# Kernel optimization log

Hardware: AMD Instinct MI355X
Metric: run time of the kernel (lower is better)

Reference implementation:

```python
import jax, jax.numpy as jnp
import numpy as np

EPS = 1e-6
TOP_K = 2


def setup_inputs() -> dict:
    key = jax.random.key(0)
    k0, k1, k2, k3, k4 = jax.random.split(key, 5)
    B, S, H, I, E = 1, 2048, 1024, 3584, 8
    return {
        "hidden_states": jax.random.normal(k0, (B, S, H), jnp.float32),
        "rms_weight": jnp.ones((H,), jnp.float32),
        "gate_w": jax.random.normal(k1, (E, H), jnp.float32) * (H ** -0.5),
        "w1": jax.random.normal(k2, (E, I, H), jnp.float32) * (H ** -0.5),
        "w2": jax.random.normal(k3, (E, H, I), jnp.float32) * (I ** -0.5),
        "w3": jax.random.normal(k4, (E, I, H), jnp.float32) * (H ** -0.5),
    }


def reference(hidden_states, rms_weight, gate_w, w1, w2, w3):
    B, S, H = hidden_states.shape
    E = gate_w.shape[0]
    # RMSNorm (fp32 internally, matches _RMSNorm)
    x = hidden_states.astype(jnp.float32)
    var = jnp.mean(x * x, axis=-1, keepdims=True)
    h = rms_weight * (x * jax.lax.rsqrt(var + EPS))  # [B,S,H]
    # Router: softmax over experts, top-k, renormalize
    logits = jnp.einsum('bsh,eh->bse', h, gate_w)
    scores = jax.nn.softmax(logits.astype(jnp.float32), axis=-1)
    top_w, top_i = jax.lax.top_k(scores, TOP_K)        # [B,S,K]
    top_w = top_w / jnp.sum(top_w, axis=-1, keepdims=True)
    top_w = top_w.astype(h.dtype)
    # Per-token combine weight for every expert: cw[t,e]
    hf = h.reshape(-1, H)                               # [T,H]
    oh = jax.nn.one_hot(top_i.reshape(-1, TOP_K), E, dtype=h.dtype)  # [T,K,E]
    cw = jnp.einsum('tke,tk->te', oh, top_w.reshape(-1, TOP_K))       # [T,E]
    # SwiGLU expert MLPs, batched over experts (dense dispatch; weights zero out unrouted tokens)
    a = jnp.einsum('th,eih->eti', hf, w1)               # [E,T,I]
    g = jnp.einsum('th,eih->eti', hf, w3)               # [E,T,I]
    eo = jnp.einsum('eti,ehi->eth', jax.nn.silu(a) * g, w2)  # [E,T,H]
    out = jnp.einsum('eth,te->th', eo, cw)              # [T,H]
    return hidden_states + out.reshape(B, S, H)
```

## Files before the change

### kernel.cpp

```cpp
#include <hip/hip_runtime.h>
#include <hip/hip_bf16.h>
#include <stdint.h>

#define T_TOK 2048
#define HDIM  1024
#define IDIM  3584
#define NEXP  8
#define NROWS 4096
#define WELEM 29360128

typedef __attribute__((ext_vector_type(8))) short bf16x8;
typedef __attribute__((ext_vector_type(4))) float f32x4;
typedef __attribute__((ext_vector_type(4))) unsigned int u32x4;

typedef __attribute__((address_space(3))) unsigned lds_u32;
typedef const __attribute__((address_space(1))) unsigned glb_u32;

#define MFMA16 __builtin_amdgcn_mfma_f32_16x16x32_bf16

__device__ __forceinline__ unsigned short f2bf(float f){
  union { float f; unsigned u; } v; v.f = f;
  unsigned r = v.u + 0x7FFFu + ((v.u >> 16) & 1u);
  return (unsigned short)(r >> 16);
}
__device__ __forceinline__ unsigned cvt2(float a, float b){
  __hip_bfloat162 h = __float22bfloat162_rn(float2{a, b});
  return *reinterpret_cast<unsigned*>(&h);
}
__device__ __forceinline__ bf16x8 pack8(float4 lo, float4 hi){
  union { __hip_bfloat162 b2[4]; bf16x8 v; } u;
  u.b2[0] = __float22bfloat162_rn(float2{lo.x, lo.y});
  u.b2[1] = __float22bfloat162_rn(float2{lo.z, lo.w});
  u.b2[2] = __float22bfloat162_rn(float2{hi.x, hi.y});
  u.b2[3] = __float22bfloat162_rn(float2{hi.z, hi.w});
  return u.v;
}

__global__ __launch_bounds__(256) void k_rms_router(
    const float* __restrict__ x, const float* __restrict__ rmsw,
    const float* __restrict__ gw, unsigned short* __restrict__ h_bf,
    int* __restrict__ topk_i, float* __restrict__ topk_w, int* __restrict__ count)
{
  const int t = blockIdx.x, tid = threadIdx.x;
  const int lane = tid & 63, wid = tid >> 6;
  float4 x4 = reinterpret_cast<const float4*>(x)[t*256 + tid];
  float ss = x4.x*x4.x + x4.y*x4.y + x4.z*x4.z + x4.w*x4.w;
  #pragma unroll
  for (int o = 32; o >= 1; o >>= 1) ss += __shfl_xor(ss, o);
  __shared__ float sred[4];
  __shared__ float slog[32];
  if (lane == 0) sred[wid] = ss;
  __syncthreads();
  float inv = rsqrtf((sred[0]+sred[1]+sred[2]+sred[3]) * (1.0f/HDIM) + 1e-6f);
  float4 w4 = reinterpret_cast<const float4*>(rmsw)[tid];
  float h0 = x4.x*inv*w4.x, h1 = x4.y*inv*w4.y, h2 = x4.z*inv*w4.z, h3 = x4.w*inv*w4.w;
  ushort4 hb; hb.x = f2bf(h0); hb.y = f2bf(h1); hb.z = f2bf(h2); hb.w = f2bf(h3);
  reinterpret_cast<ushort4*>(h_bf)[t*256 + tid] = hb;
  #pragma unroll
  for (int e = 0; e < NEXP; e++){
    float4 g4 = reinterpret_cast<const float4*>(gw)[e*256 + tid];
    float v = h0*g4.x + h1*g4.y + h2*g4.z + h3*g4.w;
    #pragma unroll
    for (int o = 32; o >= 1; o >>= 1) v += __shfl_xor(v, o);
    if (lane == 0) slog[e*4 + wid] = v;
  }
  __syncthreads();
  if (tid == 0){
    float lg[NEXP];
    #pragma unroll
    for (int e = 0; e < NEXP; e++) lg[e] = slog[e*4]+slog[e*4+1]+slog[e*4+2]+slog[e*4+3];
    int i0 = 0;
    for (int e = 1; e < NEXP; e++) if (lg[e] > lg[i0]) i0 = e;
    int i1 = -1;
    for (int e = 0; e < NEXP; e++){ if (e == i0) continue; if (i1 < 0 || lg[e] > lg[i1]) i1 = e; }
    float m  = fmaxf(lg[i0], lg[i1]);
    float e0 = expf(lg[i0]-m), e1 = expf(lg[i1]-m);
    float s  = e0 + e1;
    topk_i[t*2] = i0; topk_i[t*2+1] = i1;
    topk_w[t*2] = e0/s; topk_w[t*2+1] = e1/s;
    atomicAdd(&count[i0], 1); atomicAdd(&count[i1], 1);
  }
}

__global__ void k_scan(const int* __restrict__ count, int* __restrict__ offset){
  if (threadIdx.x == 0){
    int o = 0;
    for (int e = 0; e < NEXP; e++){ offset[e] = o; o += count[e]; }
  }
}

__global__ __launch_bounds__(256) void k_scatter(
    const int* __restrict__ topk_i, const float* __restrict__ topk_w,
    const int* __restrict__ offset, int* __restrict__ cursor,
    int* __restrict__ token_of_row, float* __restrict__ wrow, int* __restrict__ slot_of)
{
  int t = blockIdx.x*256 + threadIdx.x;
  if (t >= T_TOK) return;
  #pragma unroll
  for (int k = 0; k < 2; k++){
    int e = topk_i[t*2+k];
    int pos = atomicAdd(&cursor[e], 1);
    int row = offset[e] + pos;
    token_of_row[row] = t;
    wrow[row] = topk_w[t*2+k];
    slot_of[t*2+k] = row;
  }
}

__global__ __launch_bounds__(256) void k_cvt(
    const float4* __restrict__ src, uint2* __restrict__ dst, int n4)
{
  int stride = gridDim.x * blockDim.x;
  for (int i = blockIdx.x*blockDim.x + threadIdx.x; i < n4; i += stride){
    float4 v = src[i];
    dst[i] = make_uint2(cvt2(v.x, v.y), cvt2(v.z, v.w));
  }
}

__global__ __launch_bounds__(256, 3) void k_mlp_in_bf(
    const unsigned short* __restrict__ h_bf, const unsigned short* __restrict__ w1bf,
    const unsigned short* __restrict__ w3bf, const int* __restrict__ token_of_row,
    const int* __restrict__ count, const int* __restrict__ offset,
    unsigned short* __restrict__ act)
{
  const int d = blockIdx.x;
  const int e = d & 7;
  const int q = d >> 3;
  const int panel = q >> 4;
  const int rt = q & 15;
  const int cnt = count[e];
  if (rt * 128 >= cnt) return;
  const int off = offset[e], row0 = off + rt*128, rend = off + cnt;
  const int col0 = panel * 64;
  const int tid = threadIdx.x, lane = tid & 63, wid = tid >> 6;
  const int wave_r = wid >> 1, wave_c = wid & 1;

  __shared__ __align__(16) char sA [128*128];
  __shared__ __align__(16) char sB1[64*128];
  __shared__ __align__(16) char sB2[64*128];

  const int srow = tid >> 3;
  const int sg   = (tid & 7) ^ (srow & 7);

  const unsigned short* aptr[4];
  #pragma unroll
  for (int j = 0; j < 4; j++){
    int tok = token_of_row[min(row0 + srow + 32*j, NROWS-1)];
    aptr[j] = h_bf + (size_t)tok*HDIM + sg*8;
  }
  const unsigned short* b1ptr[2];
  const unsigned short* b3ptr[2];
  #pragma unroll
  for (int j = 0; j < 2; j++){
    int col = col0 + srow + 32*j;
    b1ptr[j] = w1bf + (size_t)(e*IDIM + col)*HDIM + sg*8;
    b3ptr[j] = w3bf + (size_t)(e*IDIM + col)*HDIM + sg*8;
  }

  #define ISSUE(kk) {                                                                \
    _Pragma("unroll")                                                                \
    for (int j = 0; j < 4; j++)                                                      \
      __builtin_amdgcn_global_load_lds((glb_u32*)(const void*)(aptr[j] + (kk)*64),   \
          (lds_u32*)(void*)(sA + j*4096 + tid*16), 16, 0, 0);                        \
    _Pragma("unroll")                                                                \
    for (int j = 0; j < 2; j++){                                                     \
      __builtin_amdgcn_global_load_lds((glb_u32*)(const void*)(b1ptr[j] + (kk)*64),  \
          (lds_u32*)(void*)(sB1 + j*4096 + tid*16), 16, 0, 0);                       \
      __builtin_amdgcn_global_load_lds((glb_u32*)(const void*)(b3ptr[j] + (kk)*64),  \
          (lds_u32*)(void*)(sB2 + j*4096 + tid*16), 16, 0, 0);                       \
    } }

  f32x4 acc1[4][2], acc3[4][2];
  #pragma unroll
  for (int m = 0; m < 4; m++)
    #pragma unroll
    for (int n = 0; n < 2; n++){
      acc1[m][n] = (f32x4){0.f,0.f,0.f,0.f};
      acc3[m][n] = (f32x4){0.f,0.f,0.f,0.f};
    }

  for (int kk = 0; kk < HDIM/64; kk++){
    ISSUE(kk);
    __syncthreads();
    #pragma unroll
    for (int ki = 0; ki < 2; ki++){
      bf16x8 af[4];
      #pragma unroll
      for (int m = 0; m < 4; m++){
        int row = wave_r*64 + m*16 + (lane & 15);
        int slot = ki*4 + (lane >> 4);
        af[m] = *reinterpret_cast<const bf16x8*>(sA + row*128 + ((slot ^ (row&7))<<4));
      }
      #pragma unroll
      for (int n = 0; n < 2; n++){
        int col = wave_c*32 + n*16 + (lane & 15);
        int slot = ki*4 + (lane >> 4);
        bf16x8 b1 = *reinterpret_cast<const bf16x8*>(sB1 + col*128 + ((slot ^ (col&7))<<4));
        bf16x8 b2 = *reinterpret_cast<const bf16x8*>(sB2 + col*128 + ((slot ^ (col&7))<<4));
        #pragma unroll
        for (int m = 0; m < 4; m++){
          acc1[m][n] = MFMA16(af[m], b1, acc1[m][n], 0,0,0);
          acc3[m][n] = MFMA16(af[m], b2, acc3[m][n], 0,0,0);
        }
      }
    }
    __syncthreads();
  }

  const int lcol = lane & 15, lrow4 = (lane >> 4) * 4;
  #pragma unroll
  for (int m = 0; m < 4; m++){
    #pragma unroll
    for (int n = 0; n < 2; n++){
      int gcol = col0 + wave_c*32 + n*16 + lcol;
      #pragma unroll
      for (int r = 0; r < 4; r++){
        int grow = row0 + wave_r*64 + m*16 + lrow4 + r;
        if (grow < rend){
          float a = acc1[m][n][r], g = acc3[m][n][r];
          float sig = 1.0f / (1.0f + __expf(-a));
          act[(size_t)grow*IDIM + gcol] = f2bf(a * sig * g);
        }
      }
    }
  }
  #undef ISSUE
}

__global__ __launch_bounds__(256, 4) void k_mlp_out_bf(
    const unsigned short* __restrict__ act, const unsigned short* __restrict__ w2bf,
    const float* __restrict__ wrow, const int* __restrict__ count,
    const int* __restrict__ offset, float* __restrict__ eo)
{
  const int d = blockIdx.x;
  const int e = d & 7;
  const int q = d >> 3;
  const int panel = q >> 4;
  const int rt = q & 15;
  const int cnt = count[e];
  if (rt * 128 >= cnt) return;
  const int off = offset[e], row0 = off + rt*128, rend = off + cnt;
  const int col0 = panel * 64;
  const int tid = threadIdx.x, lane = tid & 63, wid = tid >> 6;
  const int wave_r = wid >> 1, wave_c = wid & 1;

  __shared__ __align__(16) char sA[128*128];
  __shared__ __align__(16) char sB[64*128];

  const int srow = tid >> 3;
  const int sg   = (tid & 7) ^ (srow & 7);

  const unsigned short* aptr[4];
  #pragma unroll
  for (int j = 0; j < 4; j++){
    int r = min(row0 + srow + 32*j, NROWS-1);
    aptr[j] = act + (size_t)r*IDIM + sg*8;
  }
  const unsigned short* bptr[2];
  #pragma unroll
  for (int j = 0; j < 2; j++){
    int col = col0 + srow + 32*j;
    bptr[j] = w2bf + (size_t)(e*HDIM + col)*IDIM + sg*8;
  }

  #define ISSUE(kk) {                                                                \
    _Pragma("unroll")                                                                \
    for (int j = 0; j < 4; j++)                                                      \
      __builtin_amdgcn_global_load_lds((glb_u32*)(const void*)(aptr[j] + (kk)*64),   \
          (lds_u32*)(void*)(sA + j*4096 + tid*16), 16, 0, 0);                        \
    _Pragma("unroll")                                                                \
    for (int j = 0; j < 2; j++)                                                      \
      __builtin_amdgcn_global_load_lds((glb_u32*)(const void*)(bptr[j] + (kk)*64),   \
          (lds_u32*)(void*)(sB + j*4096 + tid*16), 16, 0, 0); }

  f32x4 acc[4][2];
  #pragma unroll
  for (int m = 0; m < 4; m++)
    #pragma unroll
    for (int n = 0; n < 2; n++) acc[m][n] = (f32x4){0.f,0.f,0.f,0.f};

  for (int kk = 0; kk < IDIM/64; kk++){
    ISSUE(kk);
    __syncthreads();
    #pragma unroll
    for (int ki = 0; ki < 2; ki++){
      bf16x8 af[4];
      #pragma unroll
      for (int m = 0; m < 4; m++){
        int row = wave_r*64 + m*16 + (lane & 15);
        int slot = ki*4 + (lane >> 4);
        af[m] = *reinterpret_cast<const bf16x8*>(sA + row*128 + ((slot ^ (row&7))<<4));
      }
      #pragma unroll
      for (int n = 0; n < 2; n++){
        int col = wave_c*32 + n*16 + (lane & 15);
        int slot = ki*4 + (lane >> 4);
        bf16x8 fb = *reinterpret_cast<const bf16x8*>(sB + col*128 + ((slot ^ (col&7))<<4));
        #pragma unroll
        for (int m = 0; m < 4; m++)
          acc[m][n] = MFMA16(af[m], fb, acc[m][n], 0,0,0);
      }
    }
    __syncthreads();
  }

  const int lcol = lane & 15, lrow4 = (lane >> 4) * 4;
  #pragma unroll
  for (int m = 0; m < 4; m++){
    #pragma unroll
    for (int n = 0; n < 2; n++){
      int gcol = col0 + wave_c*32 + n*16 + lcol;
      #pragma unroll
      for (int r = 0; r < 4; r++){
        int grow = row0 + wave_r*64 + m*16 + lrow4 + r;
        if (grow < rend){
          eo[(size_t)grow*HDIM + gcol] = acc[m][n][r] * wrow[grow];
        }
      }
    }
  }
  #undef ISSUE
}

__global__ __launch_bounds__(256, 2) void k_mlp_in_fb(
    const unsigned short* __restrict__ h_bf, const float* __restrict__ w1,
    const float* __restrict__ w3, const int* __restrict__ token_of_row,
    const int* __restrict__ count, const int* __restrict__ offset,
    unsigned short* __restrict__ act)
{
  int bx, by, bz;
  {
    int d = blockIdx.x + 16*(blockIdx.y + 56*blockIdx.z);
    int w = (d & 7)*896 + (d >> 3);
    bx = w & 15; int r = w >> 4; by = r % 56; bz = r / 56;
  }
  const int e = bz, tile = bx;
  const int cnt = count[e];
  if (tile * 128 >= cnt) return;
  const int off  = offset[e];
  const int row0 = off + tile*128;
  const int rend = off + cnt;
  const int col0 = by * 64;
  const int tid = threadIdx.x, lane = tid & 63, wid = tid >> 6;
  const int wave_r = wid >> 1, wave_c = wid & 1;

  __shared__ __align__(16) char sA [128*128];
  __shared__ __align__(16) char sB1[64*128];
  __shared__ __align__(16) char sB2[64*128];

  const int arow_base = tid >> 3;
  const int kseg = tid & 7;
  const unsigned short* aptr[4];
  #pragma unroll
  for (int j = 0; j < 4; j++){
    int r = row0 + arow_base + 32*j;
    aptr[j] = h_bf + (size_t)token_of_row[min(r, NROWS-1)]*HDIM + kseg*8;
  }
  const float* w1base = w1 + (size_t)e*IDIM*HDIM + (size_t)col0*HDIM + (size_t)arow_base*HDIM + kseg*8;
  const float* w3base = w3 + (size_t)e*IDIM*HDIM + (size_t)col0*HDIM + (size_t)arow_base*HDIM + kseg*8;

  u32x4  pa[4];
  float4 pb1[2][2], pb3[2][2];

  auto LOAD = [&](int kk){
    #pragma unroll
    for (int j = 0; j < 4; j++)
      pa[j] = *reinterpret_cast<const u32x4*>(aptr[j] + kk*64);
    #pragma unroll
    for (int j = 0; j < 2; j++){
      const float4* p1 = reinterpret_cast<const float4*>(w1base + (size_t)(32*j)*HDIM + kk*64);
      const float4* p3 = reinterpret_cast<const float4*>(w3base + (size_t)(32*j)*HDIM + kk*64);
      pb1[j][0] = p1[0]; pb1[j][1] = p1[1];
      pb3[j][0] = p3[0]; pb3[j][1] = p3[1];
    }
  };
  const int aswz = (kseg ^ (arow_base & 7)) << 4;
  auto STORE = [&](){
    #pragma unroll
    for (int j = 0; j < 4; j++)
      *reinterpret_cast<u32x4*>(sA + (arow_base + 32*j)*128 + aswz) = pa[j];
    #pragma unroll
    for (int j = 0; j < 2; j++){
      *reinterpret_cast<bf16x8*>(sB1 + (arow_base + 32*j)*128 + aswz) = pack8(pb1[j][0], pb1[j][1]);
      *reinterpret_cast<bf16x8*>(sB2 + (arow_base + 32*j)*128 + aswz) = pack8(pb3[j][0], pb3[j][1]);
    }
  };

  f32x4 acc_a[4][2], acc_g[4][2];
  #pragma unroll
  for (int m = 0; m < 4; m++)
    #pragma unroll
    for (int n = 0; n < 2; n++){
      acc_a[m][n] = (f32x4){0.f,0.f,0.f,0.f};
      acc_g[m][n] = (f32x4){0.f,0.f,0.f,0.f};
    }

  LOAD(0);
  for (int kk = 0; kk < HDIM/64; kk++){
    STORE();
    if (kk + 1 < HDIM/64) LOAD(kk+1);
    __syncthreads();
    #pragma unroll
    for (int ki = 0; ki < 2; ki++){
      bf16x8 af[4];
      #pragma unroll
      for (int m = 0; m < 4; m++){
        int row = wave_r*64 + m*16 + (lane&15);
        int slot = ki*4 + (lane>>4);
        af[m] = *reinterpret_cast<const bf16x8*>(sA + row*128 + ((slot ^ (row&7))<<4));
      }
      #pragma unroll
      for (int n = 0; n < 2; n++){
        int col = wave_c*32 + n*16 + (lane&15);
        int slot = ki*4 + (lane>>4);
        bf16x8 b1 = *reinterpret_cast<const bf16x8*>(sB1 + col*128 + ((slot ^ (col&7))<<4));
        bf16x8 b2 = *reinterpret_cast<const bf16x8*>(sB2 + col*128 + ((slot ^ (col&7))<<4));
        #pragma unroll
        for (int m = 0; m < 4; m++){
          acc_a[m][n] = MFMA16(af[m], b1, acc_a[m][n], 0,0,0);
          acc_g[m][n] = MFMA16(af[m], b2, acc_g[m][n], 0,0,0);
        }
      }
    }
    __syncthreads();
  }
  const int lcol = lane & 15, lrow4 = (lane >> 4) * 4;
  #pragma unroll
  for (int m = 0; m < 4; m++){
    #pragma unroll
    for (int n = 0; n < 2; n++){
      int gcol = col0 + wave_c*32 + n*16 + lcol;
      #pragma unroll
      for (int r = 0; r < 4; r++){
        int grow = row0 + wave_r*64 + m*16 + lrow4 + r;
        if (grow < rend){
          float a = acc_a[m][n][r], g = acc_g[m][n][r];
          float sig = 1.0f / (1.0f + __expf(-a));
          act[(size_t)grow*IDIM + gcol] = f2bf(a * sig * g);
        }
      }
    }
  }
}

__global__ __launch_bounds__(256, 3) void k_mlp_out_fb(
    const unsigned short* __restrict__ act, const float* __restrict__ w2,
    const float* __restrict__ wrow, const int* __restrict__ count,
    const int* __restrict__ offset, float* __restrict__ eo)
{
  int bx, by, bz;
  {
    int d = blockIdx.x + 16*(blockIdx.y + 16*blockIdx.z);
    int w = (d & 7)*256 + (d >> 3);
    bx = w & 15; int r = w >> 4; by = r & 15; bz = r >> 4;
  }
  const int e = bz, tile = bx;
  const int cnt = count[e];
  if (tile*128 >= cnt) return;
  const int off = offset[e], row0 = off + tile*128, rend = off + cnt;
  const int col0 = by * 64;
  const int tid = threadIdx.x, lane = tid & 63, wid = tid >> 6;
  const int wave_r = wid >> 1, wave_c = wid & 1;

  __shared__ __align__(16) char sA[128*128];
  __shared__ __align__(16) char sB[64*128];

  const int arow_base = tid >> 3, kseg = tid & 7;
  const unsigned short* aptr[4];
  #pragma unroll
  for (int j = 0; j < 4; j++){
    int r = min(row0 + arow_base + 32*j, NROWS-1);
    aptr[j] = act + (size_t)r * IDIM + kseg*8;
  }
  const float* w2base = w2 + (size_t)e*HDIM*IDIM + (size_t)col0*IDIM + (size_t)arow_base*IDIM + kseg*8;

  u32x4  pa[4];
  float4 pb[2][2];

  auto LOAD = [&](int kk){
    #pragma unroll
    for (int j = 0; j < 4; j++)
      pa[j] = *reinterpret_cast<const u32x4*>(aptr[j] + kk*64);
    #pragma unroll
    for (int j = 0; j < 2; j++){
      const float4* p = reinterpret_cast<const float4*>(w2base + (size_t)(32*j)*IDIM + kk*64);
      pb[j][0] = p[0]; pb[j][1] = p[1];
    }
  };
  const int aswz = (kseg ^ (arow_base & 7)) << 4;
  auto STORE = [&](){
    #pragma unroll
    for (int j = 0; j < 4; j++)
      *reinterpret_cast<u32x4*>(sA + (arow_base + 32*j)*128 + aswz) = pa[j];
    #pragma unroll
    for (int j = 0; j < 2; j++)
      *reinterpret_cast<bf16x8*>(sB + (arow_base + 32*j)*128 + aswz) = pack8(pb[j][0], pb[j][1]);
  };

  f32x4 acc[4][2];
  #pragma unroll
  for (int m = 0; m < 4; m++)
    #pragma unroll
    for (int n = 0; n < 2; n++) acc[m][n] = (f32x4){0.f,0.f,0.f,0.f};

  LOAD(0);
  for (int kk = 0; kk < IDIM/64; kk++){
    STORE();
    if (kk + 1 < IDIM/64) LOAD(kk+1);
    __syncthreads();
    #pragma unroll
    for (int ki = 0; ki < 2; ki++){
      bf16x8 af[4];
      #pragma unroll
      for (int m = 0; m < 4; m++){
        int row = wave_r*64 + m*16 + (lane&15);
        int slot = ki*4 + (lane>>4);
        af[m] = *reinterpret_cast<const bf16x8*>(sA + row*128 + ((slot ^ (row&7))<<4));
      }
      #pragma unroll
      for (int n = 0; n < 2; n++){
        int col = wave_c*32 + n*16 + (lane&15);
        int slot = ki*4 + (lane>>4);
        bf16x8 fb = *reinterpret_cast<const bf16x8*>(sB + col*128 + ((slot ^ (col&7))<<4));
        #pragma unroll
        for (int m = 0; m < 4; m++)
          acc[m][n] = MFMA16(af[m], fb, acc[m][n], 0,0,0);
      }
    }
    __syncthreads();
  }
  const int lcol = lane & 15, lrow4 = (lane >> 4) * 4;
  #pragma unroll
  for (int m = 0; m < 4; m++){
    #pragma unroll
    for (int n = 0; n < 2; n++){
      int gcol = col0 + wave_c*32 + n*16 + lcol;
      #pragma unroll
      for (int r = 0; r < 4; r++){
        int grow = row0 + wave_r*64 + m*16 + lrow4 + r;
        if (grow < rend){
          eo[(size_t)grow*HDIM + gcol] = acc[m][n][r] * wrow[grow];
        }
      }
    }
  }
}

__global__ __launch_bounds__(256) void k_combine(
    const float* __restrict__ x, const float* __restrict__ eo,
    const int* __restrict__ slot_of, float* __restrict__ out)
{
  const int t = blockIdx.x, tid = threadIdx.x;
  const int s0 = slot_of[t*2], s1 = slot_of[t*2+1];
  float4 xv = reinterpret_cast<const float4*>(x)[t*256 + tid];
  float4 a  = reinterpret_cast<const float4*>(eo)[s0*256 + tid];
  float4 b  = reinterpret_cast<const float4*>(eo)[s1*256 + tid];
  float4 ov;
  ov.x = xv.x + a.x + b.x;
  ov.y = xv.y + a.y + b.y;
  ov.z = xv.z + a.z + b.z;
  ov.w = xv.w + a.w + b.w;
  reinterpret_cast<float4*>(out)[t*256 + tid] = ov;
}

extern "C" void kernel_launch(void* const* d_in, const int* in_sizes, int n_in,
                              void* d_out, int out_size, void* d_ws, size_t ws_size,
                              hipStream_t stream)
{
  const float* x    = (const float*)d_in[0];
  const float* rmsw = (const float*)d_in[1];
  const float* gw   = (const float*)d_in[2];
  const float* w1   = (const float*)d_in[3];
  const float* w2   = (const float*)d_in[4];
  const float* w3   = (const float*)d_in[5];
  float* out = (float*)d_out;

  char* ws = (char*)d_ws;
  size_t o = 0;
  auto alloc = [&](size_t bytes) -> void* {
    void* p = ws + o;
    o += (bytes + 255) & ~(size_t)255;
    return p;
  };
  unsigned short* h_bf   = (unsigned short*)alloc((size_t)T_TOK*HDIM*2);
  int*   topk_i          = (int*)  alloc(T_TOK*2*4);
  float* topk_w          = (float*)alloc(T_TOK*2*4);
  int*   counters        = (int*)  alloc(64*4);
  int*   token_of_row    = (int*)  alloc(NROWS*4);
  float* wrow            = (float*)alloc(NROWS*4);
  int*   slot_of         = (int*)  alloc(T_TOK*2*4);
  unsigned short* act    = (unsigned short*)alloc((size_t)NROWS*IDIM*2);
  float* eo              = (float*)alloc((size_t)NROWS*HDIM*4);
  int* count  = counters;
  int* cursor = counters + 8;
  int* offset = counters + 16;

  const size_t wbf_bytes = (size_t)2 * WELEM * 2;
  bool bfpath = (ws_size >= o + wbf_bytes);
  unsigned short* w1bfp = (unsigned short*)(ws + o);
  unsigned short* w3bfp = w1bfp + WELEM;
  unsigned short* w2bfp = w1bfp;

  hipMemsetAsync(counters, 0, 64*4, stream);
  k_rms_router<<<T_TOK, 256, 0, stream>>>(x, rmsw, gw, h_bf, topk_i, topk_w, count);
  k_scan<<<1, 64, 0, stream>>>(count, offset);
  k_scatter<<<(T_TOK+255)/256, 256, 0, stream>>>(topk_i, topk_w, offset, cursor,
                                                 token_of_row, wrow, slot_of);
  if (bfpath){
    k_cvt<<<2048, 256, 0, stream>>>((const float4*)w1, (uint2*)w1bfp, WELEM/4);
    k_cvt<<<2048, 256, 0, stream>>>((const float4*)w3, (uint2*)w3bfp, WELEM/4);
    k_mlp_in_bf<<<7168, 256, 0, stream>>>(h_bf, w1bfp, w3bfp, token_of_row,
                                          count, offset, act);
    k_cvt<<<2048, 256, 0, stream>>>((const float4*)w2, (uint2*)w2bfp, WELEM/4);
    k_mlp_out_bf<<<2048, 256, 0, stream>>>(act, w2bfp, wrow, count, offset, eo);
  } else {
    k_mlp_in_fb <<<dim3(16, 56, 8), 256, 0, stream>>>(h_bf, w1, w3, token_of_row,
                                                      count, offset, act);
    k_mlp_out_fb<<<dim3(16, 16, 8), 256, 0, stream>>>(act, w2, wrow, count, offset, eo);
  }
  k_combine<<<T_TOK, 256, 0, stream>>>(x, eo, slot_of, out);
}
```

Before: 348.6 us.

## Double-buffer LDS tiles in bf16 expert GEMMs with prefetch two steps ahead

Both bf16 expert MLP kernels now keep two LDS buffers and issue the global-to-LDS loads for tile kk+2 while computing tile kk. Explicit vmcnt waits and raw s_barrier calls replace the two __syncthreads per iteration, so memory latency can overlap MFMA work. LDS use per block doubles and the occupancy hint drops to 2 blocks per CU, which trades latency hiding from extra waves for in-block prefetching. Correctness depends on the hand-counted vmcnt thresholds matching the number of outstanding loads.

Result: slower. 394.2 us (+13.1%).

```diff
diff --git a/kernel.cpp b/kernel.cpp
--- a/kernel.cpp
+++ b/kernel.cpp
@@ -34,6 +34,13 @@
   u.b2[2] = __float22bfloat162_rn(float2{hi.x, hi.y});
   u.b2[3] = __float22bfloat162_rn(float2{hi.z, hi.w});
   return u.v;
+}
+
+__device__ __forceinline__ void pub_barrier(){
+  asm volatile("s_waitcnt lgkmcnt(0)" ::: "memory");
+  __builtin_amdgcn_sched_barrier(0);
+  __builtin_amdgcn_s_barrier();
+  __builtin_amdgcn_sched_barrier(0);
 }
 
 __global__ __launch_bounds__(256) void k_rms_router(
@@ -117,7 +124,7 @@
   }
 }
 
-__global__ __launch_bounds__(256, 3) void k_mlp_in_bf(
+__global__ __launch_bounds__(256, 2) void k_mlp_in_bf(
     const unsigned short* __restrict__ h_bf, const unsigned short* __restrict__ w1bf,
     const unsigned short* __restrict__ w3bf, const int* __restrict__ token_of_row,
     const int* __restrict__ count, const int* __restrict__ offset,
@@ -135,9 +142,9 @@
   const int tid = threadIdx.x, lane = tid & 63, wid = tid >> 6;
   const int wave_r = wid >> 1, wave_c = wid & 1;
 
-  __shared__ __align__(16) char sA [128*128];
-  __shared__ __align__(16) char sB1[64*128];
-  __shared__ __align__(16) char sB2[64*128];
+  __shared__ __align__(16) char sA [2*16384];
+  __shared__ __align__(16) char sB1[2*8192];
+  __shared__ __align__(16) char sB2[2*8192];
 
   const int srow = tid >> 3;
   const int sg   = (tid & 7) ^ (srow & 7);
@@ -157,17 +164,17 @@
     b3ptr[j] = w3bf + (size_t)(e*IDIM + col)*HDIM + sg*8;
   }
 
-  #define ISSUE(kk) {                                                                \
+  #define ISSUE(kk, b) {                                                             \
     _Pragma("unroll")                                                                \
     for (int j = 0; j < 4; j++)                                                      \
       __builtin_amdgcn_global_load_lds((glb_u32*)(const void*)(aptr[j] + (kk)*64),   \
-          (lds_u32*)(void*)(sA + j*4096 + tid*16), 16, 0, 0);                        \
+          (lds_u32*)(void*)(sA + (b)*16384 + j*4096 + tid*16), 16, 0, 0);            \
     _Pragma("unroll")                                                                \
     for (int j = 0; j < 2; j++){                                                     \
       __builtin_amdgcn_global_load_lds((glb_u32*)(const void*)(b1ptr[j] + (kk)*64),  \
-          (lds_u32*)(void*)(sB1 + j*4096 + tid*16), 16, 0, 0);                       \
+          (lds_u32*)(void*)(sB1 + (b)*8192 + j*4096 + tid*16), 16, 0, 0);            \
       __builtin_amdgcn_global_load_lds((glb_u32*)(const void*)(b3ptr[j] + (kk)*64),  \
-          (lds_u32*)(void*)(sB2 + j*4096 + tid*16), 16, 0, 0);                       \
+          (lds_u32*)(void*)(sB2 + (b)*8192 + j*4096 + tid*16), 16, 0, 0);            \
     } }
 
   f32x4 acc1[4][2], acc3[4][2];
@@ -179,32 +186,42 @@
       acc3[m][n] = (f32x4){0.f,0.f,0.f,0.f};
     }
 
-  for (int kk = 0; kk < HDIM/64; kk++){
-    ISSUE(kk);
-    __syncthreads();
-    #pragma unroll
-    for (int ki = 0; ki < 2; ki++){
-      bf16x8 af[4];
-      #pragma unroll
-      for (int m = 0; m < 4; m++){
-        int row = wave_r*64 + m*16 + (lane & 15);
-        int slot = ki*4 + (lane >> 4);
-        af[m] = *reinterpret_cast<const bf16x8*>(sA + row*128 + ((slot ^ (row&7))<<4));
-      }
-      #pragma unroll
-      for (int n = 0; n < 2; n++){
-        int col = wave_c*32 + n*16 + (lane & 15);
-        int slot = ki*4 + (lane >> 4);
-        bf16x8 b1 = *reinterpret_cast<const bf16x8*>(sB1 + col*128 + ((slot ^ (col&7))<<4));
-        bf16x8 b2 = *reinterpret_cast<const bf16x8*>(sB2 + col*128 + ((slot ^ (col&7))<<4));
-        #pragma unroll
-        for (int m = 0; m < 4; m++){
-          acc1[m][n] = MFMA16(af[m], b1, acc1[m][n], 0,0,0);
-          acc3[m][n] = MFMA16(af[m], b2, acc3[m][n], 0,0,0);
-        }
-      }
-    }
-    __syncthreads();
+  #define COMPUTE(b) { _Pragma("unroll")                                             \
+    for (int ki = 0; ki < 2; ki++){                                                  \
+      bf16x8 af[4];                                                                  \
+      _Pragma("unroll")                                                              \
+      for (int m = 0; m < 4; m++){                                                   \
+        int row = wave_r*64 + m*16 + (lane & 15);                                    \
+        int slot = ki*4 + (lane >> 4);                                               \
+        af[m] = *reinterpret_cast<const bf16x8*>(sA + (b)*16384 + row*128 + ((slot ^ (row&7))<<4)); \
+      }                                                                              \
+      _Pragma("unroll")                                                              \
+      for (int n = 0; n < 2; n++){                                                   \
+        int col = wave_c*32 + n*16 + (lane & 15);                                    \
+        int slot = ki*4 + (lane >> 4);                                               \
+        bf16x8 b1 = *reinterpret_cast<const bf16x8*>(sB1 + (b)*8192 + col*128 + ((slot ^ (col&7))<<4)); \
+        bf16x8 b2 = *reinterpret_cast<const bf16x8*>(sB2 + (b)*8192 + col*128 + ((slot ^ (col&7))<<4)); \
+        _Pragma("unroll")                                                            \
+        for (int m = 0; m < 4; m++){                                                 \
+          acc1[m][n] = MFMA16(af[m], b1, acc1[m][n], 0,0,0);                         \
+          acc3[m][n] = MFMA16(af[m], b2, acc3[m][n], 0,0,0);                         \
+        }                                                                            \
+      }                                                                              \
+    } }
+
+  const int NK = HDIM/64;
+  ISSUE(0, 0);
+  ISSUE(1, 1);
+  for (int kk = 0; kk < NK; kk++){
+    const int b = kk & 1;
+    if (kk < NK-1){ asm volatile("s_waitcnt vmcnt(8)" ::: "memory"); }
+    else          { asm volatile("s_waitcnt vmcnt(0)" ::: "memory"); }
+    __builtin_amdgcn_sched_barrier(0);
+    __builtin_amdgcn_s_barrier();
+    __builtin_amdgcn_sched_barrier(0);
+    COMPUTE(b);
+    pub_barrier();
+    if (kk + 2 < NK) ISSUE(kk+2, b);
   }
 
   const int lcol = lane & 15, lrow4 = (lane >> 4) * 4;
@@ -225,9 +242,10 @@
     }
   }
   #undef ISSUE
-}
-
-__global__ __launch_bounds__(256, 4) void k_mlp_out_bf(
+  #undef COMPUTE
+}
+
+__global__ __launch_bounds__(256, 2) void k_mlp_out_bf(
     const unsigned short* __restrict__ act, const unsigned short* __restrict__ w2bf,
     const float* __restrict__ wrow, const int* __restrict__ count,
     const int* __restrict__ offset, float* __restrict__ eo)
@@ -244,8 +262,8 @@
   const int tid = threadIdx.x, lane = tid & 63, wid = tid >> 6;
   const int wave_r = wid >> 1, wave_c = wid & 1;
 
-  __shared__ __align__(16) char sA[128*128];
-  __shared__ __align__(16) char sB[64*128];
+  __shared__ __align__(16) char sA[2*16384];
+  __shared__ __align__(16) char sB[2*8192];
 
   const int srow = tid >> 3;
   const int sg   = (tid & 7) ^ (srow & 7);
@@ -263,15 +281,15 @@
     bptr[j] = w2bf + (size_t)(e*HDIM + col)*IDIM + sg*8;
   }
 
-  #define ISSUE(kk) {                                                                \
+  #define ISSUE(kk, b) {                                                             \
     _Pragma("unroll")                                                                \
     for (int j = 0; j < 4; j++)                                                      \
       __builtin_amdgcn_global_load_lds((glb_u32*)(const void*)(aptr[j] + (kk)*64),   \
-          (lds_u32*)(void*)(sA + j*4096 + tid*16), 16, 0, 0);                        \
+          (lds_u32*)(void*)(sA + (b)*16384 + j*4096 + tid*16), 16, 0, 0);            \
     _Pragma("unroll")                                                                \
     for (int j = 0; j < 2; j++)                                                      \
       __builtin_amdgcn_global_load_lds((glb_u32*)(const void*)(bptr[j] + (kk)*64),   \
-          (lds_u32*)(void*)(sB + j*4096 + tid*16), 16, 0, 0); }
+          (lds_u32*)(void*)(sB + (b)*8192 + j*4096 + tid*16), 16, 0, 0); }
 
   f32x4 acc[4][2];
   #pragma unroll
@@ -279,29 +297,39 @@
     #pragma unroll
     for (int n = 0; n < 2; n++) acc[m][n] = (f32x4){0.f,0.f,0.f,0.f};
 
-  for (int kk = 0; kk < IDIM/64; kk++){
-    ISSUE(kk);
-    __syncthreads();
-    #pragma unroll
-    for (int ki = 0; ki < 2; ki++){
-      bf16x8 af[4];
-      #pragma unroll
-      for (int m = 0; m < 4; m++){
-        int row = wave_r*64 + m*16 + (lane & 15);
-        int slot = ki*4 + (lane >> 4);
-        af[m] = *reinterpret_cast<const bf16x8*>(sA + row*128 + ((slot ^ (row&7))<<4));
-      }
-      #pragma unroll
-      for (int n = 0; n < 2; n++){
-        int col = wave_c*32 + n*16 + (lane & 15);
-        int slot = ki*4 + (lane >> 4);
-        bf16x8 fb = *reinterpret_cast<const bf16x8*>(sB + col*128 + ((slot ^ (col&7))<<4));
-        #pragma unroll
-        for (int m = 0; m < 4; m++)
-          acc[m][n] = MFMA16(af[m], fb, acc[m][n], 0,0,0);
-      }
-    }
-    __syncthreads();
+  #define COMPUTE(b) { _Pragma("unroll")                                             \
+    for (int ki = 0; ki < 2; ki++){                                                  \
+      bf16x8 af[4];                                                                  \
+      _Pragma("unroll")                                                              \
+      for (int m = 0; m < 4; m++){                                                   \
+        int row = wave_r*64 + m*16 + (lane & 15);                                    \
+        int slot = ki*4 + (lane >> 4);                                               \
+        af[m] = *reinterpret_cast<const bf16x8*>(sA + (b)*16384 + row*128 + ((slot ^ (row&7))<<4)); \
+      }                                                                              \
+      _Pragma("unroll")                                                              \
+      for (int n = 0; n < 2; n++){                                                   \
+        int col = wave_c*32 + n*16 + (lane & 15);                                    \
+        int slot = ki*4 + (lane >> 4);                                               \
+        bf16x8 fb = *reinterpret_cast<const bf16x8*>(sB + (b)*8192 + col*128 + ((slot ^ (col&7))<<4)); \
+        _Pragma("unroll")                                                            \
+        for (int m = 0; m < 4; m++)                                                  \
+          acc[m][n] = MFMA16(af[m], fb, acc[m][n], 0,0,0);                           \
+      }                                                                              \
+    } }
+
+  const int NK = IDIM/64;
+  ISSUE(0, 0);
+  ISSUE(1, 1);
+  for (int kk = 0; kk < NK; kk++){
+    const int b = kk & 1;
+    if (kk < NK-1){ asm volatile("s_waitcnt vmcnt(6)" ::: "memory"); }
+    else          { asm volatile("s_waitcnt vmcnt(0)" ::: "memory"); }
+    __builtin_amdgcn_sched_barrier(0);
+    __builtin_amdgcn_s_barrier();
+    __builtin_amdgcn_sched_barrier(0);
+    COMPUTE(b);
+    pub_barrier();
+    if (kk + 2 < NK) ISSUE(kk+2, b);
   }
 
   const int lcol = lane & 15, lrow4 = (lane >> 4) * 4;
@@ -320,6 +348,7 @@
     }
   }
   #undef ISSUE
+  #undef COMPUTE
 }
 
 __global__ __launch_bounds__(256, 2) void k_mlp_in_fb(
```
